# Kernel optimization log

Measured on AMD Instinct MI355X. Metric: run time of the kernel, lower is better.

## Reference

```python
import jax, jax.numpy as jnp
import numpy as np

H = 8          # n_heads
D = 1024       # dim_tgt == dim_mem
DQ = D // H    # per-head dim = 128
BN = 512       # LFFN bottleneck (hardcoded in module)
HID = 1024     # LFFN hidden (hardcoded in module)
B = 16
S_T = 1024     # target length
S_M = 2048     # memory length
SCALE = DQ ** 0.25  # module uses dim_q ** (1/4)
EPS = 1e-5


def _ln(x, g, b):
    m = jnp.mean(x, axis=-1, keepdims=True)
    v = jnp.mean(jnp.square(x - m), axis=-1, keepdims=True)
    return (x - m) * jax.lax.rsqrt(v + EPS) * g + b


def _mhla(xq, xk, xv, Wq, Wk, Wv, Wo, masked):
    # per-head projections: x [b,s,D] x W [H,D,DQ] -> [b,H,s,DQ]
    Q = jnp.einsum('bsq,hqd->bhsd', xq, Wq)
    K = jnp.einsum('bsq,hqd->bhsd', xk, Wk)
    V = jnp.einsum('bsq,hqd->bhsd', xv, Wv)
    if masked:
        s, d = Q.shape[-2], Q.shape[-1]
        # module adds log(triu(ones).T) directly to Q: 0 where d_idx<=t, -inf otherwise
        m = jnp.where(jnp.arange(d)[None, :] <= jnp.arange(s)[:, None], 0.0, -jnp.inf)
        Q = Q + m.astype(Q.dtype)
    # softmax_col(K^T/d_k) over head-dim axis == softmax(K/d_k, axis=-1)
    A = jnp.einsum('bhsd,bhse->bhde', jax.nn.softmax(K / SCALE, axis=-1), V)  # [b,H,DQ,DQ]
    Bm = jnp.einsum('bhsd,bhde->bhse', jax.nn.softmax(Q / SCALE, axis=-1), A)  # [b,H,s,DQ]
    b, h, w, dd = Bm.shape
    # torch .view(b, w, h*d) on contiguous [b,h,w,d]: raw row-major reshape (no transpose)
    Bm = Bm.reshape(b, w, h * dd)
    return Bm @ Wo.T


def setup_inputs():
    key = jax.random.key(0)
    ks = jax.random.split(key, 24)
    r = lambda k, sh, s=0.02: (jax.random.normal(k, sh, jnp.float32) * s)
    return {
        'mem': jax.random.normal(ks[0], (B, S_M, D), jnp.float32),
        'y': jax.random.normal(ks[1], (B, S_T, D), jnp.float32),
        # self-attention (masked)
        'Wq1': r(ks[2], (H, D, DQ)), 'Wk1': r(ks[3], (H, D, DQ)), 'Wv1': r(ks[4], (H, D, DQ)),
        'Wo1': r(ks[5], (D, D)),
        # cross-attention with memory
        'Wq2': r(ks[6], (H, D, DQ)), 'Wk2': r(ks[7], (H, D, DQ)), 'Wv2': r(ks[8], (H, D, DQ)),
        'Wo2': r(ks[9], (D, D)),
        # LFFN (torch Linear weights are [out, in])
        'E1': r(ks[10], (BN, D)), 'D1': r(ks[11], (HID, BN)),
        'E2': r(ks[12], (BN, HID)), 'D2': r(ks[13], (D, BN)),
        # LayerNorm affine params
        'g1': jnp.ones((D,), jnp.float32), 'b1': jnp.zeros((D,), jnp.float32),
        'g2': jnp.ones((D,), jnp.float32), 'b2': jnp.zeros((D,), jnp.float32),
        'g3': jnp.ones((D,), jnp.float32), 'b3': jnp.zeros((D,), jnp.float32),
    }


def reference(mem, y, Wq1, Wk1, Wv1, Wo1, Wq2, Wk2, Wv2, Wo2,
              E1, D1, E2, D2, g1, b1, g2, b2, g3, b3):
    # dropout layers are identity in eval mode
    y = y + _mhla(y, y, y, Wq1, Wk1, Wv1, Wo1, masked=True)
    y = _ln(y, g1, b1)
    y = y + _mhla(y, mem, mem, Wq2, Wk2, Wv2, Wo2, masked=False)
    y = _ln(y, g2, b2)
    # LFFN: E1 -> D1 -> swish -> E2 -> D2
    h = (y @ E1.T) @ D1.T
    h = h * jax.nn.sigmoid(h)
    ffn = (h @ E2.T) @ D2.T
    y = _ln(y + ffn, g3, b3)
    return y
```

## Files before the change

kernel.cpp:

```cpp
#include <hip/hip_runtime.h>
#include <hip/hip_bf16.h>

#define DEVI __device__ __forceinline__

typedef __bf16 bfrag __attribute__((ext_vector_type(8)));
typedef unsigned short us8 __attribute__((ext_vector_type(8)));
typedef float f32x4 __attribute__((ext_vector_type(4)));
typedef unsigned short ushort_t;

static constexpr int NB  = 16;
static constexpr int NH  = 8;
static constexpr int DIM = 1024;
static constexpr int DQh = 128;
static constexpr int ST  = 1024;
static constexpr int SM  = 2048;
static constexpr float INV_SCALE = 0.29730177875068026f;
static constexpr float LN_EPS = 1e-5f;

DEVI ushort_t f2bf(float f) {
  __hip_bfloat16 h = __float2bfloat16(f);
  return __builtin_bit_cast(ushort_t, h);
}
DEVI float bf2f(ushort_t u) {
  return __bfloat162float(__builtin_bit_cast(__hip_bfloat16, u));
}
DEVI bfrag ldfrag(const ushort_t* p) {
  return __builtin_bit_cast(bfrag, *(const us8*)p);
}
DEVI void gl16(const ushort_t* g, ushort_t* l) {
  __builtin_amdgcn_global_load_lds(
      (const __attribute__((address_space(1))) void*)g,
      (__attribute__((address_space(3))) void*)l, 16, 0, 0);
}

enum { ST_BF16 = 0, ST_SWISH = 1, ST_F32RES = 2, ST_SCR = 3 };

__global__ __launch_bounds__(256, 4)
void gemm_qkv(const ushort_t* __restrict__ A, const ushort_t* __restrict__ Bt,
              ushort_t* __restrict__ P0, ushort_t* __restrict__ P1,
              ushort_t* __restrict__ P2,
              int M, int N, int K, int logS, int smflags, int maskflags)
{
  __shared__ ushort_t As[128][32];
  __shared__ ushort_t Bs[128][32];
  const int tid = threadIdx.x;
  int bx = blockIdx.x, by = blockIdx.y;
  {
    const int gx = gridDim.x;
    const int nwg = gx * gridDim.y;
    int bid = by * gx + bx;
    if ((nwg & 7) == 0) bid = (bid & 7) * (nwg >> 3) + (bid >> 3);
    bx = bid % gx; by = bid / gx;
  }
  const int m0 = by * 128, n0 = bx * 128;

  const int lane = tid & 63;
  const int w = tid >> 6;
  const int wr = w * 32;
  const int frow = lane & 15;
  const int q = lane >> 4;

  const int grow = lane >> 2;
  const int gk = ((lane & 3) ^ ((lane >> 3) & 3)) * 8;
  const ushort_t* Ag = A + (long)(m0 + w * 32 + grow) * K + gk;
  const ushort_t* Bg = Bt + (long)(n0 + w * 32 + grow) * K + gk;

  f32x4 acc[2][8];
  #pragma unroll
  for (int i = 0; i < 2; ++i)
    #pragma unroll
    for (int j = 0; j < 8; ++j) acc[i][j] = f32x4{0.f, 0.f, 0.f, 0.f};

  const int kqs = (frow >> 1) & 3;
  for (int k0 = 0; k0 < K; k0 += 32) {
    __syncthreads();
    gl16(Ag + k0,                &As[w * 32][0]);
    gl16(Ag + k0 + (long)16 * K, &As[w * 32 + 16][0]);
    gl16(Bg + k0,                &Bs[w * 32][0]);
    gl16(Bg + k0 + (long)16 * K, &Bs[w * 32 + 16][0]);
    __syncthreads();
    const int kq = (q ^ kqs) * 8;
    const bfrag af0 = ldfrag(&As[wr + frow][kq]);
    const bfrag af1 = ldfrag(&As[wr + 16 + frow][kq]);
    #pragma unroll
    for (int j = 0; j < 8; ++j) {
      const bfrag bf = ldfrag(&Bs[j * 16 + frow][kq]);
      acc[0][j] = __builtin_amdgcn_mfma_f32_16x16x32_bf16(af0, bf, acc[0][j], 0, 0, 0);
      acc[1][j] = __builtin_amdgcn_mfma_f32_16x16x32_bf16(af1, bf, acc[1][j], 0, 0, 0);
    }
  }

  const int sel = n0 >> 10;
  const bool dosm   = (smflags >> sel) & 1;
  const bool domask = (maskflags >> sel) & 1;
  const int h = (n0 >> 7) & 7;
  ushort_t* __restrict__ Bq = (sel == 0) ? P0 : ((sel == 1) ? P1 : P2);
  const int S = 1 << logS;
  #pragma unroll
  for (int i = 0; i < 2; ++i) {
    #pragma unroll
    for (int e = 0; e < 4; ++e) {
      const int gm = m0 + wr + i * 16 + q * 4 + e;
      const int b = gm >> logS, s = gm & (S - 1);
      float v[8];
      #pragma unroll
      for (int j = 0; j < 8; ++j) v[j] = acc[i][j][e];
      if (dosm) {
        #pragma unroll
        for (int j = 0; j < 8; ++j) {
          v[j] *= INV_SCALE;
          if (domask && (j * 16 + frow) > s) v[j] = -3.0e38f;
        }
        float mx = v[0];
        #pragma unroll
        for (int j = 1; j < 8; ++j) mx = fmaxf(mx, v[j]);
        mx = fmaxf(mx, __shfl_xor(mx, 1));
        mx = fmaxf(mx, __shfl_xor(mx, 2));
        mx = fmaxf(mx, __shfl_xor(mx, 4));
        mx = fmaxf(mx, __shfl_xor(mx, 8));
        float sm = 0.f;
        #pragma unroll
        for (int j = 0; j < 8; ++j) { v[j] = __expf(v[j] - mx); sm += v[j]; }
        sm += __shfl_xor(sm, 1);
        sm += __shfl_xor(sm, 2);
        sm += __shfl_xor(sm, 4);
        sm += __shfl_xor(sm, 8);
        const float inv = 1.0f / sm;
        #pragma unroll
        for (int j = 0; j < 8; ++j) v[j] *= inv;
      }
      ushort_t* rowp = Bq + ((long)(h * 16 + b) * S + (long)s) * 128;
      #pragma unroll
      for (int j = 0; j < 8; ++j) rowp[j * 16 + frow] = f2bf(v[j]);
    }
  }
}

template<int STORE>
__global__ __launch_bounds__(256, 2)
void gemm_bb(const ushort_t* __restrict__ A, const ushort_t* __restrict__ Bt,
             const float* __restrict__ Res,
             ushort_t* __restrict__ P0, float* __restrict__ Cf,
             int M, int N, int K, long aZ, long bZ)
{
  __shared__ ushort_t As[128][32];
  __shared__ ushort_t Bs[128][32];
  const int tid = threadIdx.x;
  int bx = blockIdx.x, by = blockIdx.y;
  if (gridDim.z == 1) {
    const int gx = gridDim.x;
    const int nwg = gx * gridDim.y;
    int bid = by * gx + bx;
    if ((nwg & 7) == 0) bid = (bid & 7) * (nwg >> 3) + (bid >> 3);
    bx = bid % gx; by = bid / gx;
  }
  const int z = blockIdx.z;
  const int m0 = by * 128, n0 = bx * 128;
  A  += aZ * (long)z;
  Bt += bZ * (long)z;

  const int lane = tid & 63;
  const int w = tid >> 6;
  const int wr = (w >> 1) * 64, wc = (w & 1) * 64;
  const int frow = lane & 15;
  const int q = lane >> 4;

  const int grow = lane >> 2;
  const int gk = ((lane & 3) ^ ((lane >> 3) & 3)) * 8;
  const ushort_t* Ag = A + (long)(m0 + w * 32 + grow) * K + gk;
  const ushort_t* Bg = Bt + (long)(n0 + w * 32 + grow) * K + gk;

  f32x4 acc[4][4];
  #pragma unroll
  for (int i = 0; i < 4; ++i)
    #pragma unroll
    for (int j = 0; j < 4; ++j) acc[i][j] = f32x4{0.f, 0.f, 0.f, 0.f};

  const int kqs = (frow >> 1) & 3;
  for (int k0 = 0; k0 < K; k0 += 32) {
    __syncthreads();
    gl16(Ag + k0,                &As[w * 32][0]);
    gl16(Ag + k0 + (long)16 * K, &As[w * 32 + 16][0]);
    gl16(Bg + k0,                &Bs[w * 32][0]);
    gl16(Bg + k0 + (long)16 * K, &Bs[w * 32 + 16][0]);
    __syncthreads();
    const int kq = (q ^ kqs) * 8;
    bfrag af[4], bf[4];
    #pragma unroll
    for (int i = 0; i < 4; ++i) af[i] = ldfrag(&As[wr + i * 16 + frow][kq]);
    #pragma unroll
    for (int j = 0; j < 4; ++j) bf[j] = ldfrag(&Bs[wc + j * 16 + frow][kq]);
    #pragma unroll
    for (int i = 0; i < 4; ++i)
      #pragma unroll
      for (int j = 0; j < 4; ++j)
        acc[i][j] = __builtin_amdgcn_mfma_f32_16x16x32_bf16(af[i], bf[j], acc[i][j], 0, 0, 0);
  }

  const int rb = q * 4;
  #pragma unroll
  for (int i = 0; i < 4; ++i) {
    #pragma unroll
    for (int j = 0; j < 4; ++j) {
      #pragma unroll
      for (int e = 0; e < 4; ++e) {
        const int gm = m0 + wr + i * 16 + rb + e;
        const int gn = n0 + wc + j * 16 + frow;
        float val = acc[i][j][e];
        if constexpr (STORE == ST_SWISH) val = val / (1.0f + __expf(-val));
        if constexpr (STORE == ST_F32RES) {
          Cf[(long)gm * N + gn] = val + Res[(long)gm * N + gn];
        } else if constexpr (STORE == ST_SCR) {
          const int b = z & 15, hh = z >> 4;
          P0[(long)b * (ST * DIM) + (long)(hh * 128 + (gm >> 3)) * DIM +
             (gm & 7) * 128 + gn] = f2bf(val);
        } else {
          P0[(long)gm * N + gn] = f2bf(val);
        }
      }
    }
  }
}

__global__ __launch_bounds__(256, 2)
void gemm_ktv(const ushort_t* __restrict__ Kp, const ushort_t* __restrict__ Vp,
              float* __restrict__ P, int S, int SC)
{
  __shared__ ushort_t As[128][40];
  __shared__ ushort_t Bs[128][40];
  const int tid = threadIdx.x;
  const int z = blockIdx.x;
  const int ch = blockIdx.y;
  const long base = ((long)z * S + (long)ch * SC) * DQh;
  const ushort_t* Vb = Vp + base;
  const ushort_t* Kb = Kp + base;
  const int lane = tid & 63;
  const int wr = ((tid >> 6) >> 1) * 64, wc = ((tid >> 6) & 1) * 64;
  const int frow = lane & 15, fk = (lane >> 4) * 8;
  const int c = tid & 127;
  const int sr0 = tid >> 7;

  f32x4 acc[4][4];
  #pragma unroll
  for (int i = 0; i < 4; ++i)
    #pragma unroll
    for (int j = 0; j < 4; ++j) acc[i][j] = f32x4{0.f, 0.f, 0.f, 0.f};

  for (int s0 = 0; s0 < SC; s0 += 32) {
    __syncthreads();
    #pragma unroll
    for (int p = 0; p < 16; ++p) {
      const int sr = sr0 + p * 2;
      As[c][sr] = Vb[(long)(s0 + sr) * DQh + c];
      Bs[c][sr] = Kb[(long)(s0 + sr) * DQh + c];
    }
    __syncthreads();
    bfrag af[4], bfv[4];
    #pragma unroll
    for (int i = 0; i < 4; ++i) af[i]  = ldfrag(&As[wr + i * 16 + frow][fk]);
    #pragma unroll
    for (int j = 0; j < 4; ++j) bfv[j] = ldfrag(&Bs[wc + j * 16 + frow][fk]);
    #pragma unroll
    for (int i = 0; i < 4; ++i)
      #pragma unroll
      for (int j = 0; j < 4; ++j)
        acc[i][j] = __builtin_amdgcn_mfma_f32_16x16x32_bf16(af[i], bfv[j], acc[i][j], 0, 0, 0);
  }
  float* Pz = P + ((long)ch * 128 + z) * 16384;
  const int rb = (lane >> 4) * 4;
  #pragma unroll
  for (int i = 0; i < 4; ++i)
    #pragma unroll
    for (int j = 0; j < 4; ++j)
      #pragma unroll
      for (int e = 0; e < 4; ++e)
        Pz[(long)(wr + i * 16 + rb + e) * 128 + (wc + j * 16 + frow)] = acc[i][j][e];
}

__global__ __launch_bounds__(256)
void ktv_reduce(const float* __restrict__ P, ushort_t* __restrict__ AT, int nch)
{
  const long i = ((long)blockIdx.x * 256 + threadIdx.x) * 4;
  float4 s = *(const float4*)(P + i);
  for (int c = 1; c < nch; ++c) {
    const float4 v = *(const float4*)(P + (long)c * 2097152 + i);
    s.x += v.x; s.y += v.y; s.z += v.z; s.w += v.w;
  }
  ushort4 o = make_ushort4(f2bf(s.x), f2bf(s.y), f2bf(s.z), f2bf(s.w));
  *(ushort4*)(AT + i) = o;
}

__global__ __launch_bounds__(256)
void layernorm_k(const float* __restrict__ X, const float* __restrict__ G,
                 const float* __restrict__ Bta, float* __restrict__ Y,
                 ushort_t* __restrict__ Yb)
{
  const int row = blockIdx.x;
  const int t = threadIdx.x;
  const float4 v = *(const float4*)(X + (long)row * DIM + t * 4);
  float s  = v.x + v.y + v.z + v.w;
  float sq = v.x * v.x + v.y * v.y + v.z * v.z + v.w * v.w;
  #pragma unroll
  for (int o = 32; o; o >>= 1) { s += __shfl_xor(s, o); sq += __shfl_xor(sq, o); }
  __shared__ float ps[4], pq[4];
  if ((t & 63) == 0) { ps[t >> 6] = s; pq[t >> 6] = sq; }
  __syncthreads();
  s  = ps[0] + ps[1] + ps[2] + ps[3];
  sq = pq[0] + pq[1] + pq[2] + pq[3];
  const float mean = s * (1.0f / DIM);
  const float var  = sq * (1.0f / DIM) - mean * mean;
  const float rstd = rsqrtf(var + LN_EPS);
  const float4 gv = *(const float4*)(G + t * 4);
  const float4 bv = *(const float4*)(Bta + t * 4);
  float4 o;
  o.x = (v.x - mean) * rstd * gv.x + bv.x;
  o.y = (v.y - mean) * rstd * gv.y + bv.y;
  o.z = (v.z - mean) * rstd * gv.z + bv.z;
  o.w = (v.w - mean) * rstd * gv.w + bv.w;
  *(float4*)(Y + (long)row * DIM + t * 4) = o;
  if (Yb) {
    ushort4 ob = make_ushort4(f2bf(o.x), f2bf(o.y), f2bf(o.z), f2bf(o.w));
    *(ushort4*)(Yb + (long)row * DIM + t * 4) = ob;
  }
}

__global__ __launch_bounds__(256)
void transpose_cast(const float* __restrict__ W, ushort_t* __restrict__ Wt)
{
  __shared__ float tile[32][33];
  const int z = blockIdx.z;
  const int kb = blockIdx.y * 32;
  const int nb = blockIdx.x * 32;
  const float* src = W + (long)z * DIM * DQh;
  ushort_t* dst = Wt + (long)z * DIM * DQh;
  const int tx = threadIdx.x & 31;
  const int ty = threadIdx.x >> 5;
  #pragma unroll
  for (int r = 0; r < 32; r += 8)
    tile[ty + r][tx] = src[(long)(kb + ty + r) * DQh + nb + tx];
  __syncthreads();
  #pragma unroll
  for (int r = 0; r < 32; r += 8)
    dst[(long)(nb + ty + r) * DIM + kb + tx] = f2bf(tile[tx][ty + r]);
}

__global__ __launch_bounds__(256)
void cast_bf16(const float* __restrict__ X, ushort_t* __restrict__ Yq)
{
  const long i = ((long)blockIdx.x * 256 + threadIdx.x) * 4;
  const float4 v = *(const float4*)(X + i);
  ushort4 sv = make_ushort4(f2bf(v.x), f2bf(v.y), f2bf(v.z), f2bf(v.w));
  *(ushort4*)(Yq + i) = sv;
}


extern "C" void kernel_launch(void* const* d_in, const int* in_sizes, int n_in,
                              void* d_out, int out_size, void* d_ws, size_t ws_size,
                              hipStream_t stream)
{
  (void)in_sizes; (void)n_in; (void)out_size; (void)ws_size;
  const float* mem = (const float*)d_in[0];
  const float* y0  = (const float*)d_in[1];
  const float* Wq1 = (const float*)d_in[2];
  const float* Wk1 = (const float*)d_in[3];
  const float* Wv1 = (const float*)d_in[4];
  const float* Wo1 = (const float*)d_in[5];
  const float* Wq2 = (const float*)d_in[6];
  const float* Wk2 = (const float*)d_in[7];
  const float* Wv2 = (const float*)d_in[8];
  const float* Wo2 = (const float*)d_in[9];
  const float* E1  = (const float*)d_in[10];
  const float* D1  = (const float*)d_in[11];
  const float* E2  = (const float*)d_in[12];
  const float* D2  = (const float*)d_in[13];
  const float* g1  = (const float*)d_in[14];
  const float* b1  = (const float*)d_in[15];
  const float* g2  = (const float*)d_in[16];
  const float* b2  = (const float*)d_in[17];
  const float* g3  = (const float*)d_in[18];
  const float* b3  = (const float*)d_in[19];

  char* ws = (char*)d_ws;
  const size_t MB = 1ull << 20;
  ushort_t* wcat1 = (ushort_t*)(ws + 0 * MB);
  ushort_t* wkv2  = (ushort_t*)(ws + 6 * MB);
  ushort_t* wq2t  = (ushort_t*)(ws + 10 * MB);
  ushort_t* wo1b  = (ushort_t*)(ws + 12 * MB);
  ushort_t* wo2b  = (ushort_t*)(ws + 14 * MB);
  ushort_t* e1b   = (ushort_t*)(ws + 16 * MB);
  ushort_t* d1b   = (ushort_t*)(ws + 17 * MB);
  ushort_t* e2b   = (ushort_t*)(ws + 18 * MB);
  ushort_t* d2b   = (ushort_t*)(ws + 19 * MB);
  ushort_t* y0b   = (ushort_t*)(ws + 20 * MB);
  ushort_t* memb  = (ushort_t*)(ws + 52 * MB);
  ushort_t* qbuf  = (ushort_t*)(ws + 116 * MB);
  ushort_t* kbuf  = (ushort_t*)(ws + 148 * MB);
  ushort_t* vbuf  = (ushort_t*)(ws + 212 * MB);
  ushort_t* amatT = (ushort_t*)(ws + 276 * MB);
  ushort_t* attnb = (ushort_t*)(ws + 280 * MB);
  float*    ybuf  = (float*)(ws + 312 * MB);
  ushort_t* ybf   = (ushort_t*)(ws + 376 * MB);
  ushort_t* hbuf  = (ushort_t*)(ws + 408 * MB);
  float*    pbuf  = (float*)(ws + 440 * MB);
  ushort_t* bn1   = attnb;
  ushort_t* bn2   = qbuf;

  cast_bf16<<<16384, 256, 0, stream>>>(y0, y0b);
  cast_bf16<<<32768, 256, 0, stream>>>(mem, memb);
  transpose_cast<<<dim3(4, 32, 8), 256, 0, stream>>>(Wq1, wcat1);
  transpose_cast<<<dim3(4, 32, 8), 256, 0, stream>>>(Wk1, wcat1 + (1 << 20));
  transpose_cast<<<dim3(4, 32, 8), 256, 0, stream>>>(Wv1, wcat1 + (2 << 20));
  transpose_cast<<<dim3(4, 32, 8), 256, 0, stream>>>(Wk2, wkv2);
  transpose_cast<<<dim3(4, 32, 8), 256, 0, stream>>>(Wv2, wkv2 + (1 << 20));
  transpose_cast<<<dim3(4, 32, 8), 256, 0, stream>>>(Wq2, wq2t);
  cast_bf16<<<1024, 256, 0, stream>>>(Wo1, wo1b);
  cast_bf16<<<1024, 256, 0, stream>>>(Wo2, wo2b);
  cast_bf16<<<512, 256, 0, stream>>>(E1, e1b);
  cast_bf16<<<512, 256, 0, stream>>>(D1, d1b);
  cast_bf16<<<512, 256, 0, stream>>>(E2, e2b);
  cast_bf16<<<512, 256, 0, stream>>>(D2, d2b);

  gemm_qkv<<<dim3(24, 128), 256, 0, stream>>>(
      y0b, wcat1, qbuf, kbuf, vbuf, NB * ST, 3072, DIM,
      10,  0b011,  0b001);
  gemm_ktv<<<dim3(128, 2), 256, 0, stream>>>(kbuf, vbuf, pbuf, ST, 512);
  ktv_reduce<<<2048, 256, 0, stream>>>(pbuf, amatT, 2);
  gemm_bb<ST_SCR><<<dim3(1, 8, 128), 256, 0, stream>>>(
      qbuf, amatT, nullptr, attnb, nullptr, ST, DQh, DQh, (long)ST * DQh, 16384);
  gemm_bb<ST_F32RES><<<dim3(8, 128, 1), 256, 0, stream>>>(
      attnb, wo1b, y0, nullptr, ybuf, NB * ST, DIM, DIM, 0, 0);
  layernorm_k<<<NB * ST, 256, 0, stream>>>(ybuf, g1, b1, ybuf, ybf);

  gemm_qkv<<<dim3(8, 128), 256, 0, stream>>>(
      ybf, wq2t, qbuf, nullptr, nullptr, NB * ST, 1024, DIM, 10, 0b001, 0);
  gemm_qkv<<<dim3(16, 256), 256, 0, stream>>>(
      memb, wkv2, kbuf, vbuf, nullptr, NB * SM, 2048, DIM, 11, 0b001, 0);
  gemm_ktv<<<dim3(128, 4), 256, 0, stream>>>(kbuf, vbuf, pbuf, SM, 512);
  ktv_reduce<<<2048, 256, 0, stream>>>(pbuf, amatT, 4);
  gemm_bb<ST_SCR><<<dim3(1, 8, 128), 256, 0, stream>>>(
      qbuf, amatT, nullptr, attnb, nullptr, ST, DQh, DQh, (long)ST * DQh, 16384);
  gemm_bb<ST_F32RES><<<dim3(8, 128, 1), 256, 0, stream>>>(
      attnb, wo2b, ybuf, nullptr, ybuf, NB * ST, DIM, DIM, 0, 0);
  layernorm_k<<<NB * ST, 256, 0, stream>>>(ybuf, g2, b2, ybuf, ybf);

  gemm_bb<ST_BF16><<<dim3(4, 128, 1), 256, 0, stream>>>(
      ybf, e1b, nullptr, bn1, nullptr, NB * ST, 512, DIM, 0, 0);
  gemm_bb<ST_SWISH><<<dim3(8, 128, 1), 256, 0, stream>>>(
      bn1, d1b, nullptr, hbuf, nullptr, NB * ST, DIM, 512, 0, 0);
  gemm_bb<ST_BF16><<<dim3(4, 128, 1), 256, 0, stream>>>(
      hbuf, e2b, nullptr, bn2, nullptr, NB * ST, 512, DIM, 0, 0);
  gemm_bb<ST_F32RES><<<dim3(8, 128, 1), 256, 0, stream>>>(
      bn2, d2b, ybuf, nullptr, ybuf, NB * ST, DIM, 512, 0, 0);
  layernorm_k<<<NB * ST, 256, 0, stream>>>(ybuf, g3, b3, (float*)d_out, nullptr);
}
```

Measured before the change: 871.6 us.

## Fuse Q projection, softmax and Q·A product into one kernel

Adds a fused_qa kernel that computes the per-head Q projection, applies the optional causal mask and row softmax, stages the probabilities in shared memory, and multiplies by the precomputed K^T V matrix, writing straight into the scrambled attention layout. This removes the Q buffer round-trip through global memory and the separate batched ST_SCR GEMM launch, for both self- and cross-attention. Each block now uses extra LDS (32KB for the P tile), which lowers occupancy, and the K/V projection is split from Q.

Result: no change. 868.3 us (-0.4%).

```diff
diff --git a/kernel.cpp b/kernel.cpp
--- a/kernel.cpp
+++ b/kernel.cpp
@@ -33,13 +33,12 @@
       (__attribute__((address_space(3))) void*)l, 16, 0, 0);
 }
 
-enum { ST_BF16 = 0, ST_SWISH = 1, ST_F32RES = 2, ST_SCR = 3 };
+enum { ST_BF16 = 0, ST_SWISH = 1, ST_F32RES = 2 };
 
 __global__ __launch_bounds__(256, 4)
 void gemm_qkv(const ushort_t* __restrict__ A, const ushort_t* __restrict__ Bt,
               ushort_t* __restrict__ P0, ushort_t* __restrict__ P1,
-              ushort_t* __restrict__ P2,
-              int M, int N, int K, int logS, int smflags, int maskflags)
+              int M, int N, int K, int logS, int smflags)
 {
   __shared__ ushort_t As[128][32];
   __shared__ ushort_t Bs[128][32];
@@ -91,10 +90,9 @@
   }
 
   const int sel = n0 >> 10;
-  const bool dosm   = (smflags >> sel) & 1;
-  const bool domask = (maskflags >> sel) & 1;
+  const bool dosm = (smflags >> sel) & 1;
   const int h = (n0 >> 7) & 7;
-  ushort_t* __restrict__ Bq = (sel == 0) ? P0 : ((sel == 1) ? P1 : P2);
+  ushort_t* __restrict__ Bq = (sel == 0) ? P0 : P1;
   const int S = 1 << logS;
   #pragma unroll
   for (int i = 0; i < 2; ++i) {
@@ -107,10 +105,7 @@
       for (int j = 0; j < 8; ++j) v[j] = acc[i][j][e];
       if (dosm) {
         #pragma unroll
-        for (int j = 0; j < 8; ++j) {
-          v[j] *= INV_SCALE;
-          if (domask && (j * 16 + frow) > s) v[j] = -3.0e38f;
-        }
+        for (int j = 0; j < 8; ++j) v[j] *= INV_SCALE;
         float mx = v[0];
         #pragma unroll
         for (int j = 1; j < 8; ++j) mx = fmaxf(mx, v[j]);
@@ -136,28 +131,156 @@
   }
 }
 
+template<bool MASKED>
+__global__ __launch_bounds__(256, 3)
+void fused_qa(const ushort_t* __restrict__ A, const ushort_t* __restrict__ Wq,
+              const ushort_t* __restrict__ AT, ushort_t* __restrict__ Out)
+{
+  __shared__ ushort_t As[128][32];
+  __shared__ ushort_t Bs[128][32];
+  __shared__ ushort_t Ps[4][32][128];
+  const int tid = threadIdx.x;
+  int h = blockIdx.x, by = blockIdx.y;
+  {
+    const int gx = gridDim.x;
+    const int nwg = gx * gridDim.y;
+    int bid = by * gx + h;
+    if ((nwg & 7) == 0) bid = (bid & 7) * (nwg >> 3) + (bid >> 3);
+    h = bid % gx; by = bid / gx;
+  }
+  const int m0 = by * 128;
+
+  const int lane = tid & 63;
+  const int w = tid >> 6;
+  const int wr = w * 32;
+  const int frow = lane & 15;
+  const int q = lane >> 4;
+
+  const int grow = lane >> 2;
+  const int gk = ((lane & 3) ^ ((lane >> 3) & 3)) * 8;
+  const ushort_t* Ag = A + (long)(m0 + w * 32 + grow) * 1024 + gk;
+  const ushort_t* Bg = Wq + (long)(h * 128 + w * 32 + grow) * 1024 + gk;
+
+  f32x4 acc[2][8];
+  #pragma unroll
+  for (int i = 0; i < 2; ++i)
+    #pragma unroll
+    for (int j = 0; j < 8; ++j) acc[i][j] = f32x4{0.f, 0.f, 0.f, 0.f};
+
+  const int kqs = (frow >> 1) & 3;
+  for (int k0 = 0; k0 < 1024; k0 += 32) {
+    __syncthreads();
+    gl16(Ag + k0,             &As[w * 32][0]);
+    gl16(Ag + k0 + 16 * 1024, &As[w * 32 + 16][0]);
+    gl16(Bg + k0,             &Bs[w * 32][0]);
+    gl16(Bg + k0 + 16 * 1024, &Bs[w * 32 + 16][0]);
+    __syncthreads();
+    const int kq = (q ^ kqs) * 8;
+    const bfrag af0 = ldfrag(&As[wr + frow][kq]);
+    const bfrag af1 = ldfrag(&As[wr + 16 + frow][kq]);
+    #pragma unroll
+    for (int j = 0; j < 8; ++j) {
+      const bfrag bf = ldfrag(&Bs[j * 16 + frow][kq]);
+      acc[0][j] = __builtin_amdgcn_mfma_f32_16x16x32_bf16(af0, bf, acc[0][j], 0, 0, 0);
+      acc[1][j] = __builtin_amdgcn_mfma_f32_16x16x32_bf16(af1, bf, acc[1][j], 0, 0, 0);
+    }
+  }
+
+  #pragma unroll
+  for (int i = 0; i < 2; ++i) {
+    #pragma unroll
+    for (int e = 0; e < 4; ++e) {
+      const int row32 = i * 16 + q * 4 + e;
+      const int srow = (m0 + wr + row32) & (ST - 1);
+      float v[8];
+      #pragma unroll
+      for (int j = 0; j < 8; ++j) {
+        v[j] = acc[i][j][e] * INV_SCALE;
+        if (MASKED && (j * 16 + frow) > srow) v[j] = -3.0e38f;
+      }
+      float mx = v[0];
+      #pragma unroll
+      for (int j = 1; j < 8; ++j) mx = fmaxf(mx, v[j]);
+      mx = fmaxf(mx, __shfl_xor(mx, 1));
+      mx = fmaxf(mx, __shfl_xor(mx, 2));
+      mx = fmaxf(mx, __shfl_xor(mx, 4));
+      mx = fmaxf(mx, __shfl_xor(mx, 8));
+      float sm = 0.f;
+      #pragma unroll
+      for (int j = 0; j < 8; ++j) { v[j] = __expf(v[j] - mx); sm += v[j]; }
+      sm += __shfl_xor(sm, 1);
+      sm += __shfl_xor(sm, 2);
+      sm += __shfl_xor(sm, 4);
+      sm += __shfl_xor(sm, 8);
+      const float inv = 1.0f / sm;
+      const int sw = (row32 >> 1) & 3;
+      ushort_t* pr = &Ps[w][row32][0];
+      #pragma unroll
+      for (int j = 0; j < 8; ++j) {
+        const int c = j * 16 + frow;
+        const int pos = (c & ~31) | ((((c >> 3) & 3) ^ sw) << 3) | (c & 7);
+        pr[pos] = f2bf(v[j] * inv);
+      }
+    }
+  }
+
+  f32x4 acc2[2][8];
+  #pragma unroll
+  for (int i = 0; i < 2; ++i)
+    #pragma unroll
+    for (int j = 0; j < 8; ++j) acc2[i][j] = f32x4{0.f, 0.f, 0.f, 0.f};
+
+  const ushort_t* Atg = AT + (long)((h << 4) + (m0 >> 10)) * 16384 +
+                        (long)(w * 32 + grow) * 128 + gk;
+  for (int d0 = 0; d0 < 128; d0 += 32) {
+    __syncthreads();
+    gl16(Atg + d0,            &Bs[w * 32][0]);
+    gl16(Atg + d0 + 16 * 128, &Bs[w * 32 + 16][0]);
+    __syncthreads();
+    const int kq = (q ^ kqs) * 8;
+    const bfrag af0 = ldfrag(&Ps[w][frow][d0 + kq]);
+    const bfrag af1 = ldfrag(&Ps[w][16 + frow][d0 + kq]);
+    #pragma unroll
+    for (int j = 0; j < 8; ++j) {
+      const bfrag bf = ldfrag(&Bs[j * 16 + frow][kq]);
+      acc2[0][j] = __builtin_amdgcn_mfma_f32_16x16x32_bf16(af0, bf, acc2[0][j], 0, 0, 0);
+      acc2[1][j] = __builtin_amdgcn_mfma_f32_16x16x32_bf16(af1, bf, acc2[1][j], 0, 0, 0);
+    }
+  }
+
+  ushort_t* ob = Out + (long)(m0 >> 10) * (ST * DIM);
+  #pragma unroll
+  for (int i = 0; i < 2; ++i) {
+    #pragma unroll
+    for (int e = 0; e < 4; ++e) {
+      const int srow = (m0 + wr + i * 16 + q * 4 + e) & (ST - 1);
+      ushort_t* orow = ob + (long)(h * 128 + (srow >> 3)) * DIM + (srow & 7) * 128;
+      #pragma unroll
+      for (int j = 0; j < 8; ++j)
+        orow[j * 16 + frow] = f2bf(acc2[i][j][e]);
+    }
+  }
+}
+
 template<int STORE>
 __global__ __launch_bounds__(256, 2)
 void gemm_bb(const ushort_t* __restrict__ A, const ushort_t* __restrict__ Bt,
              const float* __restrict__ Res,
              ushort_t* __restrict__ P0, float* __restrict__ Cf,
-             int M, int N, int K, long aZ, long bZ)
+             int M, int N, int K)
 {
   __shared__ ushort_t As[128][32];
   __shared__ ushort_t Bs[128][32];
   const int tid = threadIdx.x;
   int bx = blockIdx.x, by = blockIdx.y;
-  if (gridDim.z == 1) {
+  {
     const int gx = gridDim.x;
     const int nwg = gx * gridDim.y;
     int bid = by * gx + bx;
     if ((nwg & 7) == 0) bid = (bid & 7) * (nwg >> 3) + (bid >> 3);
     bx = bid % gx; by = bid / gx;
   }
-  const int z = blockIdx.z;
   const int m0 = by * 128, n0 = bx * 128;
-  A  += aZ * (long)z;
-  Bt += bZ * (long)z;
 
   const int lane = tid & 63;
   const int w = tid >> 6;
@@ -210,10 +333,6 @@
         if constexpr (STORE == ST_SWISH) val = val / (1.0f + __expf(-val));
         if constexpr (STORE == ST_F32RES) {
           Cf[(long)gm * N + gn] = val + Res[(long)gm * N + gn];
-        } else if constexpr (STORE == ST_SCR) {
-          const int b = z & 15, hh = z >> 4;
-          P0[(long)b * (ST * DIM) + (long)(hh * 128 + (gm >> 3)) * DIM +
-             (gm & 7) * 128 + gn] = f2bf(val);
         } else {
           P0[(long)gm * N + gn] = f2bf(val);
         }
@@ -382,7 +501,8 @@
 
   char* ws = (char*)d_ws;
   const size_t MB = 1ull << 20;
-  ushort_t* wcat1 = (ushort_t*)(ws + 0 * MB);
+  ushort_t* wkv1  = (ushort_t*)(ws + 0 * MB);
+  ushort_t* wq1t  = (ushort_t*)(ws + 4 * MB);
   ushort_t* wkv2  = (ushort_t*)(ws + 6 * MB);
   ushort_t* wq2t  = (ushort_t*)(ws + 10 * MB);
   ushort_t* wo1b  = (ushort_t*)(ws + 12 * MB);
@@ -393,7 +513,7 @@
   ushort_t* d2b   = (ushort_t*)(ws + 19 * MB);
   ushort_t* y0b   = (ushort_t*)(ws + 20 * MB);
   ushort_t* memb  = (ushort_t*)(ws + 52 * MB);
-  ushort_t* qbuf  = (ushort_t*)(ws + 116 * MB);
+  ushort_t* bn2   = (ushort_t*)(ws + 116 * MB);
   ushort_t* kbuf  = (ushort_t*)(ws + 148 * MB);
   ushort_t* vbuf  = (ushort_t*)(ws + 212 * MB);
   ushort_t* amatT = (ushort_t*)(ws + 276 * MB);
@@ -403,13 +523,12 @@
   ushort_t* hbuf  = (ushort_t*)(ws + 408 * MB);
   float*    pbuf  = (float*)(ws + 440 * MB);
   ushort_t* bn1   = attnb;
-  ushort_t* bn2   = qbuf;
 
   cast_bf16<<<16384, 256, 0, stream>>>(y0, y0b);
   cast_bf16<<<32768, 256, 0, stream>>>(mem, memb);
-  transpose_cast<<<dim3(4, 32, 8), 256, 0, stream>>>(Wq1, wcat1);
-  transpose_cast<<<dim3(4, 32, 8), 256, 0, stream>>>(Wk1, wcat1 + (1 << 20));
-  transpose_cast<<<dim3(4, 32, 8), 256, 0, stream>>>(Wv1, wcat1 + (2 << 20));
+  transpose_cast<<<dim3(4, 32, 8), 256, 0, stream>>>(Wk1, wkv1);
+  transpose_cast<<<dim3(4, 32, 8), 256, 0, stream>>>(Wv1, wkv1 + (1 << 20));
+  transpose_cast<<<dim3(4, 32, 8), 256, 0, stream>>>(Wq1, wq1t);
   transpose_cast<<<dim3(4, 32, 8), 256, 0, stream>>>(Wk2, wkv2);
   transpose_cast<<<dim3(4, 32, 8), 256, 0, stream>>>(Wv2, wkv2 + (1 << 20));
   transpose_cast<<<dim3(4, 32, 8), 256, 0, stream>>>(Wq2, wq2t);
@@ -420,36 +539,31 @@
   cast_bf16<<<512, 256, 0, stream>>>(E2, e2b);
   cast_bf16<<<512, 256, 0, stream>>>(D2, d2b);
 
-  gemm_qkv<<<dim3(24, 128), 256, 0, stream>>>(
-      y0b, wcat1, qbuf, kbuf, vbuf, NB * ST, 3072, DIM,
-      10,  0b011,  0b001);
+  gemm_qkv<<<dim3(16, 128), 256, 0, stream>>>(
+      y0b, wkv1, kbuf, vbuf, NB * ST, 2048, DIM, 10,  0b01);
   gemm_ktv<<<dim3(128, 2), 256, 0, stream>>>(kbuf, vbuf, pbuf, ST, 512);
   ktv_reduce<<<2048, 256, 0, stream>>>(pbuf, amatT, 2);
-  gemm_bb<ST_SCR><<<dim3(1, 8, 128), 256, 0, stream>>>(
-      qbuf, amatT, nullptr, attnb, nullptr, ST, DQh, DQh, (long)ST * DQh, 16384);
-  gemm_bb<ST_F32RES><<<dim3(8, 128, 1), 256, 0, stream>>>(
-      attnb, wo1b, y0, nullptr, ybuf, NB * ST, DIM, DIM, 0, 0);
+  fused_qa<true><<<dim3(8, 128), 256, 0, stream>>>(y0b, wq1t, amatT, attnb);
+  gemm_bb<ST_F32RES><<<dim3(8, 128), 256, 0, stream>>>(
+      attnb, wo1b, y0, nullptr, ybuf, NB * ST, DIM, DIM);
   layernorm_k<<<NB * ST, 256, 0, stream>>>(ybuf, g1, b1, ybuf, ybf);
 
-  gemm_qkv<<<dim3(8, 128), 256, 0, stream>>>(
-      ybf, wq2t, qbuf, nullptr, nullptr, NB * ST, 1024, DIM, 10, 0b001, 0);
   gemm_qkv<<<dim3(16, 256), 256, 0, stream>>>(
-      memb, wkv2, kbuf, vbuf, nullptr, NB * SM, 2048, DIM, 11, 0b001, 0);
+      memb, wkv2, kbuf, vbuf, NB * SM, 2048, DIM, 11, 0b01);
   gemm_ktv<<<dim3(128, 4), 256, 0, stream>>>(kbuf, vbuf, pbuf, SM, 512);
   ktv_reduce<<<2048, 256, 0, stream>>>(pbuf, amatT, 4);
-  gemm_bb<ST_SCR><<<dim3(1, 8, 128), 256, 0, stream>>>(
-      qbuf, amatT, nullptr, attnb, nullptr, ST, DQh, DQh, (long)ST * DQh, 16384);
-  gemm_bb<ST_F32RES><<<dim3(8, 128, 1), 256, 0, stream>>>(
-      attnb, wo2b, ybuf, nullptr, ybuf, NB * ST, DIM, DIM, 0, 0);
+  fused_qa<false><<<dim3(8, 128), 256, 0, stream>>>(ybf, wq2t, amatT, attnb);
+  gemm_bb<ST_F32RES><<<dim3(8, 128), 256, 0, stream>>>(
+      attnb, wo2b, ybuf, nullptr, ybuf, NB * ST, DIM, DIM);
   layernorm_k<<<NB * ST, 256, 0, stream>>>(ybuf, g2, b2, ybuf, ybf);
 
-  gemm_bb<ST_BF16><<<dim3(4, 128, 1), 256, 0, stream>>>(
-      ybf, e1b, nullptr, bn1, nullptr, NB * ST, 512, DIM, 0, 0);
-  gemm_bb<ST_SWISH><<<dim3(8, 128, 1), 256, 0, stream>>>(
-      bn1, d1b, nullptr, hbuf, nullptr, NB * ST, DIM, 512, 0, 0);
-  gemm_bb<ST_BF16><<<dim3(4, 128, 1), 256, 0, stream>>>(
-      hbuf, e2b, nullptr, bn2, nullptr, NB * ST, 512, DIM, 0, 0);
-  gemm_bb<ST_F32RES><<<dim3(8, 128, 1), 256, 0, stream>>>(
-      bn2, d2b, ybuf, nullptr, ybuf, NB * ST, DIM, 512, 0, 0);
+  gemm_bb<ST_BF16><<<dim3(4, 128), 256, 0, stream>>>(
+      ybf, e1b, nullptr, bn1, nullptr, NB * ST, 512, DIM);
+  gemm_bb<ST_SWISH><<<dim3(8, 128), 256, 0, stream>>>(
+      bn1, d1b, nullptr, hbuf, nullptr, NB * ST, DIM, 512);
+  gemm_bb<ST_BF16><<<dim3(4, 128), 256, 0, stream>>>(
+      hbuf, e2b, nullptr, bn2, nullptr, NB * ST, 512, DIM);
+  gemm_bb<ST_F32RES><<<dim3(8, 128), 256, 0, stream>>>(
+      bn2, d2b, ybuf, nullptr, ybuf, NB * ST, DIM, 512);
   layernorm_k<<<NB * ST, 256, 0, stream>>>(ybuf, g3, b3, (float*)d_out, nullptr);
 }
```
